# Performance work log

Measured on AMD Instinct MI355X. Metric: run time of the kernel, lower is better.

## Reference

```python
import jax, jax.numpy as jnp
import numpy as np

N_NODES = 50000

# DGL ChebConv with k=2 and the standard lambda_max=2 approximation:
#   L_hat = L - I = -D^{-1/2} A D^{-1/2}
#   X0 = X ; X1 = L_hat @ X ; out = concat([X0, X1], -1) @ W + b
# Norm uses in-degrees (DGL behavior).

def setup_inputs() -> dict:
    key = jax.random.key(0)
    ks = jax.random.split(key, 8)
    E = 800000
    src = jax.random.randint(ks[0], (E,), 0, N_NODES, dtype=jnp.int32)
    dst = jax.random.randint(ks[1], (E,), 0, N_NODES, dtype=jnp.int32)
    def w(k, shape):
        fan_in = shape[0]
        return jax.random.normal(k, shape, jnp.float32) * (1.0 / np.sqrt(fan_in))
    return {
        "x": jax.random.normal(ks[2], (N_NODES, 128), jnp.float32),
        "src": src, "dst": dst,
        "W1": w(ks[3], (256, 256)), "b1": jnp.zeros((256,), jnp.float32),
        "W2": w(ks[4], (512, 256)), "b2": jnp.zeros((256,), jnp.float32),
        "W3": w(ks[5], (512, 128)), "b3": jnp.zeros((128,), jnp.float32),
    }

def _cheb_layer(h, src, dst, dinv, W, b):
    # X1 = -D^{-1/2} A D^{-1/2} h  (lambda_max = 2)
    hn = h * dinv[:, None]
    agg = jax.ops.segment_sum(hn[src], dst, num_segments=N_NODES)
    x1 = -(agg * dinv[:, None])
    return jnp.concatenate([h, x1], axis=-1) @ W + b

def reference(x, src, dst, W1, b1, W2, b2, W3, b3):
    deg = jax.ops.segment_sum(jnp.ones_like(dst, dtype=x.dtype), dst,
                              num_segments=N_NODES)
    dinv = jnp.where(deg > 0, jax.lax.rsqrt(jnp.maximum(deg, 1.0)), 0.0)
    h = jnp.tanh(_cheb_layer(x, src, dst, dinv, W1, b1))
    for _ in range(3):  # hid_layer = 3
        h = jnp.tanh(_cheb_layer(h, src, dst, dinv, W2, b2))
    return _cheb_layer(h, src, dst, dinv, W3, b3)
```

## Files before the change

kernel.cpp:

```cpp
#include <hip/hip_runtime.h>
#include <cmath>

#define NN 50000
#define CAP 64

typedef short v8s __attribute__((ext_vector_type(8)));
typedef float v4f __attribute__((ext_vector_type(4)));

__device__ __forceinline__ float b2f(unsigned short u) {
    return __uint_as_float(((unsigned int)u) << 16);
}
__device__ __forceinline__ unsigned short f2b(float f) {
    unsigned int x = __float_as_uint(f);
    x += 0x7fffu + ((x >> 16) & 1u);
    return (unsigned short)(x >> 16);
}

__device__ __forceinline__ void gld16(const void* g, void* l) {
    __builtin_amdgcn_global_load_lds(
        (const __attribute__((address_space(1))) unsigned int*)g,
        (__attribute__((address_space(3))) unsigned int*)l, 16, 0, 0);
}

__global__ void sniff_kernel(const unsigned short* __restrict__ x, int* __restrict__ mode) {
    if (threadIdx.x == 0 && blockIdx.x == 0) {
        int c = 0;
        for (int i = 0; i < 128; ++i) {
            unsigned int e = (x[i] >> 7) & 0xFFu;
            if (e >= 100u && e <= 140u) ++c;
        }
        *mode = (c >= 112) ? 0 : 1;
    }
}

__global__ void fill_kernel(const int* __restrict__ src, const int* __restrict__ dst,
                            int* __restrict__ cnt, unsigned short* __restrict__ ell, int E) {
    int e = blockIdx.x * blockDim.x + threadIdx.x;
    if (e < E) {
        int d = dst[e];
        int pos = atomicAdd(&cnt[d], 1);
        if (pos < CAP) ell[d * CAP + pos] = (unsigned short)src[e];
    }
}

__global__ void dinv_kernel(const int* __restrict__ cnt, float* __restrict__ dinv, int n) {
    int i = blockIdx.x * blockDim.x + threadIdx.x;
    if (i < n) {
        int d = cnt[i];
        dinv[i] = (d > 0) ? rsqrtf((float)d) : 0.0f;
    }
}

__global__ void prep_kernel(const void* __restrict__ x,
                            const void* __restrict__ W1, const void* __restrict__ W2,
                            const void* __restrict__ W3, const void* __restrict__ b1,
                            const void* __restrict__ b2, const void* __restrict__ b3,
                            unsigned short* __restrict__ buf,
                            unsigned short* __restrict__ WT1, unsigned short* __restrict__ WT2,
                            unsigned short* __restrict__ WT3, unsigned short* __restrict__ bb1,
                            unsigned short* __restrict__ bb2, unsigned short* __restrict__ bb3,
                            const int* __restrict__ modep) {
    int mode = *modep;
    int b = blockIdx.x, t = threadIdx.x;
    if (b < 3125) {
        int idx = b * 256 + t;
        int n = idx >> 4, c = idx & 15;
        if (mode == 0) {
            ((uint4*)buf)[n * 64 + c] = ((const uint4*)x)[idx];
        } else {
            const float* xf = (const float*)x + (size_t)idx * 8;
            unsigned short o[8];
#pragma unroll
            for (int i = 0; i < 8; ++i) o[i] = f2b(xf[i]);
            ((uint4*)buf)[n * 64 + c] = *(const uint4*)o;
        }
    } else if (b < 3381) {
        int idx = (b - 3125) * 256 + t;
        int n = idx >> 8, k = idx & 255;
        WT1[idx] = mode ? f2b(((const float*)W1)[k * 256 + n])
                        : ((const unsigned short*)W1)[k * 256 + n];
    } else if (b < 3893) {
        int idx = (b - 3381) * 256 + t;
        int n = idx >> 9, k = idx & 511;
        WT2[idx] = mode ? f2b(((const float*)W2)[k * 256 + n])
                        : ((const unsigned short*)W2)[k * 256 + n];
    } else if (b < 4149) {
        int idx = (b - 3893) * 256 + t;
        int n = idx >> 9, k = idx & 511;
        WT3[idx] = mode ? f2b(((const float*)W3)[k * 128 + n])
                        : ((const unsigned short*)W3)[k * 128 + n];
    } else {
        if (t < 256) {
            bb1[t] = mode ? f2b(((const float*)b1)[t]) : ((const unsigned short*)b1)[t];
            bb2[t] = mode ? f2b(((const float*)b2)[t]) : ((const unsigned short*)b2)[t];
        }
        if (t < 128)
            bb3[t] = mode ? f2b(((const float*)b3)[t]) : ((const unsigned short*)b3)[t];
    }
}

template <int FPL>
__global__ void spmm_kernel(const unsigned short* __restrict__ h, int ldh,
                            const int* __restrict__ cnt, const unsigned short* __restrict__ ell,
                            const float* __restrict__ dinv,
                            unsigned short* __restrict__ out, int ldo) {
    int node = blockIdx.x * 4 + (threadIdx.x >> 6);
    int lane = threadIdx.x & 63;
    int c = cnt[node]; c = (c < CAP) ? c : CAP;
    int sl = (int)ell[node * CAP + lane];
    float dl = dinv[sl];
    float acc[FPL];
#pragma unroll
    for (int i = 0; i < FPL; ++i) acc[i] = 0.f;
    const int col = lane * FPL;

    int g = 0;
    for (; g + 8 <= c; g += 8) {
        int s[8]; float d[8];
#pragma unroll
        for (int i = 0; i < 8; ++i) { s[i] = __shfl(sl, g + i); d[i] = __shfl(dl, g + i); }
        if (FPL == 4) {
            ushort4 v[8];
#pragma unroll
            for (int i = 0; i < 8; ++i)
                v[i] = *(const ushort4*)(h + (size_t)s[i] * ldh + col);
#pragma unroll
            for (int i = 0; i < 8; ++i) {
                acc[0] += d[i] * b2f(v[i].x); acc[1] += d[i] * b2f(v[i].y);
                acc[2] += d[i] * b2f(v[i].z); acc[3] += d[i] * b2f(v[i].w);
            }
        } else {
            ushort2 v[8];
#pragma unroll
            for (int i = 0; i < 8; ++i)
                v[i] = *(const ushort2*)(h + (size_t)s[i] * ldh + col);
#pragma unroll
            for (int i = 0; i < 8; ++i) {
                acc[0] += d[i] * b2f(v[i].x); acc[1] += d[i] * b2f(v[i].y);
            }
        }
    }
    for (; g < c; ++g) {
        int sg = __shfl(sl, g);
        float dg = __shfl(dl, g);
        const unsigned short* hp = h + (size_t)sg * ldh + col;
        if (FPL == 4) {
            ushort4 v = *(const ushort4*)hp;
            acc[0] += dg * b2f(v.x); acc[1] += dg * b2f(v.y);
            acc[2] += dg * b2f(v.z); acc[3] += dg * b2f(v.w);
        } else {
            ushort2 v = *(const ushort2*)hp;
            acc[0] += dg * b2f(v.x); acc[1] += dg * b2f(v.y);
        }
    }

    float dn = -dinv[node];
    unsigned short* op = out + (size_t)node * ldo + col;
    if (FPL == 4) {
        ushort4 o;
        o.x = f2b(acc[0] * dn); o.y = f2b(acc[1] * dn);
        o.z = f2b(acc[2] * dn); o.w = f2b(acc[3] * dn);
        *(ushort4*)op = o;
    } else {
        ushort2 o;
        o.x = f2b(acc[0] * dn); o.y = f2b(acc[1] * dn);
        *(ushort2*)op = o;
    }
}

template <int K32, int NQ>
__global__ void gemm_lds_kernel(const unsigned short* __restrict__ A, int lda,
                                const unsigned short* __restrict__ WT,
                                const unsigned short* __restrict__ bias,
                                void* __restrict__ out, int ldo,
                                int M, int dotanh, int is_final, const int* __restrict__ modep) {
    constexpr int K    = K32 * 32;
    constexpr int NB   = NQ * 64;
    constexpr int NTHR = 2 * NQ * 64;
    constexpr int ACH  = 128 * 4;
    constexpr int BCH  = NB * 4;
    constexpr int ROUNDS = (ACH + BCH) / NTHR;
    __shared__ unsigned short lds[(128 + NB) * 32];

    const int tid = threadIdx.x;
    const int wave = tid >> 6, lane = tid & 63, quad = lane >> 4, l16 = lane & 15;
    const int mh = wave / NQ, nq = wave % NQ;
    const int m0 = blockIdx.x * 128;

    v4f acc[4][4];
#pragma unroll
    for (int mi = 0; mi < 4; ++mi)
#pragma unroll
        for (int ni = 0; ni < 4; ++ni) acc[mi][ni] = (v4f){0.f, 0.f, 0.f, 0.f};

    const unsigned short* gp[ROUNDS];
#pragma unroll
    for (int r = 0; r < ROUNDS; ++r) {
        int c = tid + r * NTHR;
        if (c < ACH) {
            int row = m0 + (c >> 2);
            if (row >= M) row = M - 1;
            gp[r] = A + (size_t)row * lda + (c & 3) * 8;
        } else {
            int cb = c - ACH;
            gp[r] = WT + (size_t)(cb >> 2) * K + (cb & 3) * 8;
        }
    }

    const unsigned short* aT = lds;
    const unsigned short* bT = lds + 128 * 32;

    for (int k0 = 0; k0 < K; k0 += 32) {
#pragma unroll
        for (int r = 0; r < ROUNDS; ++r) {
            int c = tid + r * NTHR;
            gld16(gp[r] + k0, (void*)&lds[c * 8]);
        }
        __syncthreads();

        v8s a_frag[4], b_frag[4];
#pragma unroll
        for (int mi = 0; mi < 4; ++mi)
            a_frag[mi] = *(const v8s*)&aT[(mh * 64 + mi * 16 + l16) * 32 + quad * 8];
#pragma unroll
        for (int ni = 0; ni < 4; ++ni)
            b_frag[ni] = *(const v8s*)&bT[(nq * 64 + ni * 16 + l16) * 32 + quad * 8];
#pragma unroll
        for (int mi = 0; mi < 4; ++mi)
#pragma unroll
            for (int ni = 0; ni < 4; ++ni)
                acc[mi][ni] = __builtin_amdgcn_mfma_f32_16x16x32_bf16(a_frag[mi], b_frag[ni],
                                                                      acc[mi][ni], 0, 0, 0);
        __syncthreads();
    }

    int fin = is_final ? *modep : 0;
#pragma unroll
    for (int ni = 0; ni < 4; ++ni) {
        int colc = nq * 64 + ni * 16 + l16;
        float bv = b2f(bias[colc]);
#pragma unroll
        for (int mi = 0; mi < 4; ++mi) {
#pragma unroll
            for (int r = 0; r < 4; ++r) {
                int row = m0 + mh * 64 + mi * 16 + quad * 4 + r;
                if (row < M) {
                    float v = acc[mi][ni][r] + bv;
                    if (dotanh) v = tanhf(v);
                    if (fin) ((float*)out)[(size_t)row * ldo + colc] = v;
                    else     ((unsigned short*)out)[(size_t)row * ldo + colc] = f2b(v);
                }
            }
        }
    }
}

static inline size_t al256(size_t x) { return (x + 255) & ~(size_t)255; }

extern "C" void kernel_launch(void* const* d_in, const int* in_sizes, int n_in,
                              void* d_out, int out_size, void* d_ws, size_t ws_size,
                              hipStream_t stream) {
    const void* x  = d_in[0];
    const int* src = (const int*)d_in[1];
    const int* dst = (const int*)d_in[2];
    const void* W1 = d_in[3]; const void* b1 = d_in[4];
    const void* W2 = d_in[5]; const void* b2 = d_in[6];
    const void* W3 = d_in[7]; const void* b3 = d_in[8];
    const int E = in_sizes[1];

    char* p = (char*)d_ws;
    int* mode     = (int*)p;            p += 256;
    int* cnt      = (int*)p;            p += al256((size_t)NN * 4);
    float* dinv   = (float*)p;          p += al256((size_t)NN * 4);
    unsigned short* ell = (unsigned short*)p; p += al256((size_t)NN * CAP * 2);
    unsigned short* WT1 = (unsigned short*)p; p += al256((size_t)256 * 256 * 2);
    unsigned short* WT2 = (unsigned short*)p; p += al256((size_t)256 * 512 * 2);
    unsigned short* WT3 = (unsigned short*)p; p += al256((size_t)128 * 512 * 2);
    unsigned short* bb1 = (unsigned short*)p; p += al256((size_t)256 * 2);
    unsigned short* bb2 = (unsigned short*)p; p += al256((size_t)256 * 2);
    unsigned short* bb3 = (unsigned short*)p; p += al256((size_t)128 * 2);
    unsigned short* buf = (unsigned short*)p; p += al256((size_t)NN * 512 * 2);

    hipMemsetAsync(cnt, 0, (size_t)NN * 4, stream);
    sniff_kernel<<<1, 64, 0, stream>>>((const unsigned short*)x, mode);
    prep_kernel<<<4150, 256, 0, stream>>>(x, W1, W2, W3, b1, b2, b3,
                                          buf, WT1, WT2, WT3, bb1, bb2, bb3, mode);
    int eb = (E + 255) / 256;
    fill_kernel<<<eb, 256, 0, stream>>>(src, dst, cnt, ell, E);
    dinv_kernel<<<(NN + 255) / 256, 256, 0, stream>>>(cnt, dinv, NN);

    const int SPMM_GRID = NN / 4;
    const int GB = (NN + 127) / 128;

    spmm_kernel<2><<<SPMM_GRID, 256, 0, stream>>>(buf, 512, cnt, ell, dinv, buf + 128, 512);
    gemm_lds_kernel<8, 4><<<GB, 512, 0, stream>>>(buf, 512, WT1, bb1, buf, 512, NN, 1, 0, mode);
    spmm_kernel<4><<<SPMM_GRID, 256, 0, stream>>>(buf, 512, cnt, ell, dinv, buf + 256, 512);
    gemm_lds_kernel<16, 4><<<GB, 512, 0, stream>>>(buf, 512, WT2, bb2, buf, 512, NN, 1, 0, mode);
    spmm_kernel<4><<<SPMM_GRID, 256, 0, stream>>>(buf, 512, cnt, ell, dinv, buf + 256, 512);
    gemm_lds_kernel<16, 4><<<GB, 512, 0, stream>>>(buf, 512, WT2, bb2, buf, 512, NN, 1, 0, mode);
    spmm_kernel<4><<<SPMM_GRID, 256, 0, stream>>>(buf, 512, cnt, ell, dinv, buf + 256, 512);
    gemm_lds_kernel<16, 4><<<GB, 512, 0, stream>>>(buf, 512, WT2, bb2, buf, 512, NN, 1, 0, mode);
    spmm_kernel<4><<<SPMM_GRID, 256, 0, stream>>>(buf, 512, cnt, ell, dinv, buf + 256, 512);
    gemm_lds_kernel<16, 2><<<GB, 256, 0, stream>>>(buf, 512, WT3, bb3, d_out, 128, NN, 0, 1, mode);
}
```

Before: 555.6 us.

## Split SpMM across column slices and drop LDS staging in GEMM

The SpMM now launches several blocks per node group, each handling a 32-column slice. Lanes are split into four edge groups with a shuffle reduction at the end, which gives more parallelism and narrower gathers per block. The GEMM drops LDS staging via global_load_lds and the per-k-step barriers. Each wave now loads its MFMA fragments straight from global memory into registers, with smaller 256-thread blocks and a 64-row tile for the hidden layers. This trades LDS reuse across waves for fewer syncs, and it risks redundant global and L2 traffic since each wave reloads B and A fragments.

```diff
diff --git a/kernel.cpp b/kernel.cpp
--- a/kernel.cpp
+++ b/kernel.cpp
@@ -14,12 +14,6 @@
     unsigned int x = __float_as_uint(f);
     x += 0x7fffu + ((x >> 16) & 1u);
     return (unsigned short)(x >> 16);
-}
-
-__device__ __forceinline__ void gld16(const void* g, void* l) {
-    __builtin_amdgcn_global_load_lds(
-        (const __attribute__((address_space(1))) unsigned int*)g,
-        (__attribute__((address_space(3))) unsigned int*)l, 16, 0, 0);
 }
 
 __global__ void sniff_kernel(const unsigned short* __restrict__ x, int* __restrict__ mode) {
@@ -99,93 +93,66 @@
     }
 }
 
-template <int FPL>
-__global__ void spmm_kernel(const unsigned short* __restrict__ h, int ldh,
-                            const int* __restrict__ cnt, const unsigned short* __restrict__ ell,
+template <int NS, int OBASE>
+__global__ void spmm_kernel(const unsigned short* __restrict__ h,
+                            const int* __restrict__ cnt,
+                            const unsigned short* __restrict__ ell,
                             const float* __restrict__ dinv,
-                            unsigned short* __restrict__ out, int ldo) {
-    int node = blockIdx.x * 4 + (threadIdx.x >> 6);
-    int lane = threadIdx.x & 63;
+                            unsigned short* __restrict__ out) {
+    const int s = blockIdx.x % NS;
+    const int node = (blockIdx.x / NS) * 4 + (threadIdx.x >> 6);
+    const int lane = threadIdx.x & 63;
+    const int e = lane >> 4, cp = lane & 15;
     int c = cnt[node]; c = (c < CAP) ? c : CAP;
-    int sl = (int)ell[node * CAP + lane];
-    float dl = dinv[sl];
-    float acc[FPL];
-#pragma unroll
-    for (int i = 0; i < FPL; ++i) acc[i] = 0.f;
-    const int col = lane * FPL;
-
-    int g = 0;
-    for (; g + 8 <= c; g += 8) {
-        int s[8]; float d[8];
-#pragma unroll
-        for (int i = 0; i < 8; ++i) { s[i] = __shfl(sl, g + i); d[i] = __shfl(dl, g + i); }
-        if (FPL == 4) {
-            ushort4 v[8];
-#pragma unroll
-            for (int i = 0; i < 8; ++i)
-                v[i] = *(const ushort4*)(h + (size_t)s[i] * ldh + col);
-#pragma unroll
-            for (int i = 0; i < 8; ++i) {
-                acc[0] += d[i] * b2f(v[i].x); acc[1] += d[i] * b2f(v[i].y);
-                acc[2] += d[i] * b2f(v[i].z); acc[3] += d[i] * b2f(v[i].w);
-            }
-        } else {
-            ushort2 v[8];
-#pragma unroll
-            for (int i = 0; i < 8; ++i)
-                v[i] = *(const ushort2*)(h + (size_t)s[i] * ldh + col);
-#pragma unroll
-            for (int i = 0; i < 8; ++i) {
-                acc[0] += d[i] * b2f(v[i].x); acc[1] += d[i] * b2f(v[i].y);
-            }
-        }
-    }
-    for (; g < c; ++g) {
-        int sg = __shfl(sl, g);
-        float dg = __shfl(dl, g);
-        const unsigned short* hp = h + (size_t)sg * ldh + col;
-        if (FPL == 4) {
-            ushort4 v = *(const ushort4*)hp;
-            acc[0] += dg * b2f(v.x); acc[1] += dg * b2f(v.y);
-            acc[2] += dg * b2f(v.z); acc[3] += dg * b2f(v.w);
-        } else {
-            ushort2 v = *(const ushort2*)hp;
-            acc[0] += dg * b2f(v.x); acc[1] += dg * b2f(v.y);
-        }
-    }
-
-    float dn = -dinv[node];
-    unsigned short* op = out + (size_t)node * ldo + col;
-    if (FPL == 4) {
-        ushort4 o;
-        o.x = f2b(acc[0] * dn); o.y = f2b(acc[1] * dn);
-        o.z = f2b(acc[2] * dn); o.w = f2b(acc[3] * dn);
-        *(ushort4*)op = o;
-    } else {
-        ushort2 o;
-        o.x = f2b(acc[0] * dn); o.y = f2b(acc[1] * dn);
-        *(ushort2*)op = o;
-    }
-}
-
-template <int K32, int NQ>
-__global__ void gemm_lds_kernel(const unsigned short* __restrict__ A, int lda,
-                                const unsigned short* __restrict__ WT,
-                                const unsigned short* __restrict__ bias,
-                                void* __restrict__ out, int ldo,
-                                int M, int dotanh, int is_final, const int* __restrict__ modep) {
-    constexpr int K    = K32 * 32;
-    constexpr int NB   = NQ * 64;
-    constexpr int NTHR = 2 * NQ * 64;
-    constexpr int ACH  = 128 * 4;
-    constexpr int BCH  = NB * 4;
-    constexpr int ROUNDS = (ACH + BCH) / NTHR;
-    __shared__ unsigned short lds[(128 + NB) * 32];
-
+    int sl = 0; float dl = 0.f;
+    if (lane < c) { sl = (int)ell[node * CAP + lane]; dl = dinv[sl]; }
+    const int colb = s * 32 + cp * 2;
+    float a0 = 0.f, a1 = 0.f;
+    const int cpad = (c + 7) & ~7;
+    for (int g = 0; g < cpad; g += 8) {
+        int i0 = g + e, i1 = g + 4 + e;
+        int s0 = __shfl(sl, i0), s1 = __shfl(sl, i1);
+        float d0 = __shfl(dl, i0), d1 = __shfl(dl, i1);
+        ushort2 v0 = *(const ushort2*)(h + (size_t)s0 * 512 + colb);
+        ushort2 v1 = *(const ushort2*)(h + (size_t)s1 * 512 + colb);
+        a0 += d0 * b2f(v0.x) + d1 * b2f(v1.x);
+        a1 += d0 * b2f(v0.y) + d1 * b2f(v1.y);
+    }
+    a0 += __shfl_xor(a0, 16); a0 += __shfl_xor(a0, 32);
+    a1 += __shfl_xor(a1, 16); a1 += __shfl_xor(a1, 32);
+    if (lane < 16) {
+        float dn = -dinv[node];
+        ushort2 o; o.x = f2b(a0 * dn); o.y = f2b(a1 * dn);
+        *(ushort2*)(out + (size_t)node * 512 + OBASE + colb) = o;
+    }
+}
+
+template <int K32, int NT>
+__global__ __launch_bounds__(256) void gemm_kernel(
+        const unsigned short* __restrict__ A, int lda,
+        const unsigned short* __restrict__ WT,
+        const unsigned short* __restrict__ bias,
+        void* __restrict__ out, int ldo,
+        int M, int dotanh, int is_final, const int* __restrict__ modep) {
+    constexpr int K = K32 * 32;
+    constexpr int RPB = (4 / NT) * 64;
     const int tid = threadIdx.x;
     const int wave = tid >> 6, lane = tid & 63, quad = lane >> 4, l16 = lane & 15;
-    const int mh = wave / NQ, nq = wave % NQ;
-    const int m0 = blockIdx.x * 128;
+    const int mrow = wave / NT, nq = wave % NT;
+    const int m0 = blockIdx.x * RPB + mrow * 64;
+    const int n0 = nq * 64;
+
+    const unsigned short* Ap[4];
+#pragma unroll
+    for (int mi = 0; mi < 4; ++mi) {
+        int r = m0 + mi * 16 + l16;
+        if (r >= M) r = M - 1;
+        Ap[mi] = A + (size_t)r * lda + quad * 8;
+    }
+    const unsigned short* Bp[4];
+#pragma unroll
+    for (int ni = 0; ni < 4; ++ni)
+        Bp[ni] = WT + (size_t)(n0 + ni * 16 + l16) * K + quad * 8;
 
     v4f acc[4][4];
 #pragma unroll
@@ -193,57 +160,33 @@
 #pragma unroll
         for (int ni = 0; ni < 4; ++ni) acc[mi][ni] = (v4f){0.f, 0.f, 0.f, 0.f};
 
-    const unsigned short* gp[ROUNDS];
-#pragma unroll
-    for (int r = 0; r < ROUNDS; ++r) {
-        int c = tid + r * NTHR;
-        if (c < ACH) {
-            int row = m0 + (c >> 2);
-            if (row >= M) row = M - 1;
-            gp[r] = A + (size_t)row * lda + (c & 3) * 8;
-        } else {
-            int cb = c - ACH;
-            gp[r] = WT + (size_t)(cb >> 2) * K + (cb & 3) * 8;
-        }
-    }
-
-    const unsigned short* aT = lds;
-    const unsigned short* bT = lds + 128 * 32;
-
-    for (int k0 = 0; k0 < K; k0 += 32) {
-#pragma unroll
-        for (int r = 0; r < ROUNDS; ++r) {
-            int c = tid + r * NTHR;
-            gld16(gp[r] + k0, (void*)&lds[c * 8]);
-        }
-        __syncthreads();
-
-        v8s a_frag[4], b_frag[4];
+#pragma unroll 2
+    for (int j = 0; j < K32; ++j) {
+        v8s a[4], b[4];
+#pragma unroll
+        for (int mi = 0; mi < 4; ++mi) a[mi] = *(const v8s*)(Ap[mi] + j * 32);
+#pragma unroll
+        for (int ni = 0; ni < 4; ++ni) b[ni] = *(const v8s*)(Bp[ni] + j * 32);
 #pragma unroll
         for (int mi = 0; mi < 4; ++mi)
-            a_frag[mi] = *(const v8s*)&aT[(mh * 64 + mi * 16 + l16) * 32 + quad * 8];
-#pragma unroll
-        for (int ni = 0; ni < 4; ++ni)
-            b_frag[ni] = *(const v8s*)&bT[(nq * 64 + ni * 16 + l16) * 32 + quad * 8];
-#pragma unroll
-        for (int mi = 0; mi < 4; ++mi)
 #pragma unroll
             for (int ni = 0; ni < 4; ++ni)
-                acc[mi][ni] = __builtin_amdgcn_mfma_f32_16x16x32_bf16(a_frag[mi], b_frag[ni],
+                acc[mi][ni] = __builtin_amdgcn_mfma_f32_16x16x32_bf16(a[mi], b[ni],
                                                                       acc[mi][ni], 0, 0, 0);
-        __syncthreads();
-    }
+    }
+
+    __syncthreads();
 
     int fin = is_final ? *modep : 0;
 #pragma unroll
     for (int ni = 0; ni < 4; ++ni) {
-        int colc = nq * 64 + ni * 16 + l16;
+        int colc = n0 + ni * 16 + l16;
         float bv = b2f(bias[colc]);
 #pragma unroll
         for (int mi = 0; mi < 4; ++mi) {
 #pragma unroll
             for (int r = 0; r < 4; ++r) {
-                int row = m0 + mh * 64 + mi * 16 + quad * 4 + r;
+                int row = m0 + mi * 16 + quad * 4 + r;
                 if (row < M) {
                     float v = acc[mi][ni][r] + bv;
                     if (dotanh) v = tanhf(v);
@@ -289,17 +232,19 @@
     fill_kernel<<<eb, 256, 0, stream>>>(src, dst, cnt, ell, E);
     dinv_kernel<<<(NN + 255) / 256, 256, 0, stream>>>(cnt, dinv, NN);
 
-    const int SPMM_GRID = NN / 4;
-    const int GB = (NN + 127) / 128;
-
-    spmm_kernel<2><<<SPMM_GRID, 256, 0, stream>>>(buf, 512, cnt, ell, dinv, buf + 128, 512);
-    gemm_lds_kernel<8, 4><<<GB, 512, 0, stream>>>(buf, 512, WT1, bb1, buf, 512, NN, 1, 0, mode);
-    spmm_kernel<4><<<SPMM_GRID, 256, 0, stream>>>(buf, 512, cnt, ell, dinv, buf + 256, 512);
-    gemm_lds_kernel<16, 4><<<GB, 512, 0, stream>>>(buf, 512, WT2, bb2, buf, 512, NN, 1, 0, mode);
-    spmm_kernel<4><<<SPMM_GRID, 256, 0, stream>>>(buf, 512, cnt, ell, dinv, buf + 256, 512);
-    gemm_lds_kernel<16, 4><<<GB, 512, 0, stream>>>(buf, 512, WT2, bb2, buf, 512, NN, 1, 0, mode);
-    spmm_kernel<4><<<SPMM_GRID, 256, 0, stream>>>(buf, 512, cnt, ell, dinv, buf + 256, 512);
-    gemm_lds_kernel<16, 4><<<GB, 512, 0, stream>>>(buf, 512, WT2, bb2, buf, 512, NN, 1, 0, mode);
-    spmm_kernel<4><<<SPMM_GRID, 256, 0, stream>>>(buf, 512, cnt, ell, dinv, buf + 256, 512);
-    gemm_lds_kernel<16, 2><<<GB, 256, 0, stream>>>(buf, 512, WT3, bb3, d_out, 128, NN, 0, 1, mode);
-}
+    const int SG1 = 4 * (NN / 4);
+    const int SG  = 8 * (NN / 4);
+    const int GB4 = (NN + 63) / 64;
+    const int GB2 = (NN + 127) / 128;
+
+    spmm_kernel<4, 128><<<SG1, 256, 0, stream>>>(buf, cnt, ell, dinv, buf);
+    gemm_kernel<8, 4><<<GB4, 256, 0, stream>>>(buf, 512, WT1, bb1, buf, 512, NN, 1, 0, mode);
+    spmm_kernel<8, 256><<<SG, 256, 0, stream>>>(buf, cnt, ell, dinv, buf);
+    gemm_kernel<16, 4><<<GB4, 256, 0, stream>>>(buf, 512, WT2, bb2, buf, 512, NN, 1, 0, mode);
+    spmm_kernel<8, 256><<<SG, 256, 0, stream>>>(buf, cnt, ell, dinv, buf);
+    gemm_kernel<16, 4><<<GB4, 256, 0, stream>>>(buf, 512, WT2, bb2, buf, 512, NN, 1, 0, mode);
+    spmm_kernel<8, 256><<<SG, 256, 0, stream>>>(buf, cnt, ell, dinv, buf);
+    gemm_kernel<16, 4><<<GB4, 256, 0, stream>>>(buf, 512, WT2, bb2, buf, 512, NN, 1, 0, mode);
+    spmm_kernel<8, 256><<<SG, 256, 0, stream>>>(buf, cnt, ell, dinv, buf);
+    gemm_kernel<16, 2><<<GB2, 256, 0, stream>>>(buf, 512, WT3, bb3, d_out, 128, NN, 0, 1, mode);
+}
```

Result: slower. 1.073 ms (+93.1%).

## Stage full-K A rows in padded LDS and stream weights directly from global

Applied to the files above, without the earlier changes.

Replaces the k-stepped LDS GEMM with one that loads a 64-row block of A across the whole K dimension into padded LDS once, with a single barrier. Each wave then reads its B fragments straight from global memory (L2/L1-cached weights) instead of staging them in LDS. The M tile drops from 128 to 64 rows and each wave owns a 64-column slice. This removes the per-k-step barriers and the async global-to-LDS copies. In exchange the grid doubles, each weight fragment is re-read from cache by more blocks, and the LDS footprint grows for K=512, which may limit occupancy.

```diff
diff --git a/kernel.cpp b/kernel.cpp
--- a/kernel.cpp
+++ b/kernel.cpp
@@ -14,12 +14,6 @@
     unsigned int x = __float_as_uint(f);
     x += 0x7fffu + ((x >> 16) & 1u);
     return (unsigned short)(x >> 16);
-}
-
-__device__ __forceinline__ void gld16(const void* g, void* l) {
-    __builtin_amdgcn_global_load_lds(
-        (const __attribute__((address_space(1))) unsigned int*)g,
-        (__attribute__((address_space(3))) unsigned int*)l, 16, 0, 0);
 }
 
 __global__ void sniff_kernel(const unsigned short* __restrict__ x, int* __restrict__ mode) {
@@ -168,82 +162,73 @@
     }
 }
 
-template <int K32, int NQ>
-__global__ void gemm_lds_kernel(const unsigned short* __restrict__ A, int lda,
-                                const unsigned short* __restrict__ WT,
-                                const unsigned short* __restrict__ bias,
-                                void* __restrict__ out, int ldo,
-                                int M, int dotanh, int is_final, const int* __restrict__ modep) {
+template <int K32, int NT>
+__global__ void gemm_kernel(
+        const unsigned short* __restrict__ A, int lda,
+        const unsigned short* __restrict__ WT,
+        const unsigned short* __restrict__ bias,
+        void* __restrict__ out, int ldo,
+        int M, int dotanh, int is_final, const int* __restrict__ modep) {
     constexpr int K    = K32 * 32;
-    constexpr int NB   = NQ * 64;
-    constexpr int NTHR = 2 * NQ * 64;
-    constexpr int ACH  = 128 * 4;
-    constexpr int BCH  = NB * 4;
-    constexpr int ROUNDS = (ACH + BCH) / NTHR;
-    __shared__ unsigned short lds[(128 + NB) * 32];
+    constexpr int LDK  = K + 8;
+    constexpr int NTHR = NT * 64;
+    constexpr int CPR  = K / 8;
+    constexpr int ROUNDS = 64 * CPR / NTHR;
+    __shared__ unsigned short aT[64 * LDK];
 
     const int tid = threadIdx.x;
     const int wave = tid >> 6, lane = tid & 63, quad = lane >> 4, l16 = lane & 15;
-    const int mh = wave / NQ, nq = wave % NQ;
-    const int m0 = blockIdx.x * 128;
-
-    v4f acc[4][4];
-#pragma unroll
-    for (int mi = 0; mi < 4; ++mi)
-#pragma unroll
-        for (int ni = 0; ni < 4; ++ni) acc[mi][ni] = (v4f){0.f, 0.f, 0.f, 0.f};
-
-    const unsigned short* gp[ROUNDS];
+    const int m0 = blockIdx.x * 64;
+    const int n0 = wave * 64;
+
 #pragma unroll
     for (int r = 0; r < ROUNDS; ++r) {
         int c = tid + r * NTHR;
-        if (c < ACH) {
-            int row = m0 + (c >> 2);
-            if (row >= M) row = M - 1;
-            gp[r] = A + (size_t)row * lda + (c & 3) * 8;
-        } else {
-            int cb = c - ACH;
-            gp[r] = WT + (size_t)(cb >> 2) * K + (cb & 3) * 8;
-        }
-    }
-
-    const unsigned short* aT = lds;
-    const unsigned short* bT = lds + 128 * 32;
-
-    for (int k0 = 0; k0 < K; k0 += 32) {
-#pragma unroll
-        for (int r = 0; r < ROUNDS; ++r) {
-            int c = tid + r * NTHR;
-            gld16(gp[r] + k0, (void*)&lds[c * 8]);
-        }
-        __syncthreads();
-
-        v8s a_frag[4], b_frag[4];
+        int row = c / CPR, ko = (c % CPR) * 8;
+        int grow = m0 + row;
+        if (grow >= M) grow = M - 1;
+        v8s v = *(const v8s*)(A + (size_t)grow * lda + ko);
+        *(v8s*)&aT[row * LDK + ko] = v;
+    }
+    __syncthreads();
+
+    const unsigned short* Bp[4];
+#pragma unroll
+    for (int ni = 0; ni < 4; ++ni)
+        Bp[ni] = WT + (size_t)(n0 + ni * 16 + l16) * K + quad * 8;
+
+    v4f acc[4][4];
+#pragma unroll
+    for (int mi = 0; mi < 4; ++mi)
+#pragma unroll
+        for (int ni = 0; ni < 4; ++ni) acc[mi][ni] = (v4f){0.f, 0.f, 0.f, 0.f};
+
+#pragma unroll 4
+    for (int j = 0; j < K32; ++j) {
+        v8s a[4], b[4];
+#pragma unroll
+        for (int ni = 0; ni < 4; ++ni) b[ni] = *(const v8s*)(Bp[ni] + j * 32);
 #pragma unroll
         for (int mi = 0; mi < 4; ++mi)
-            a_frag[mi] = *(const v8s*)&aT[(mh * 64 + mi * 16 + l16) * 32 + quad * 8];
-#pragma unroll
-        for (int ni = 0; ni < 4; ++ni)
-            b_frag[ni] = *(const v8s*)&bT[(nq * 64 + ni * 16 + l16) * 32 + quad * 8];
+            a[mi] = *(const v8s*)&aT[(mi * 16 + l16) * LDK + j * 32 + quad * 8];
 #pragma unroll
         for (int mi = 0; mi < 4; ++mi)
 #pragma unroll
             for (int ni = 0; ni < 4; ++ni)
-                acc[mi][ni] = __builtin_amdgcn_mfma_f32_16x16x32_bf16(a_frag[mi], b_frag[ni],
+                acc[mi][ni] = __builtin_amdgcn_mfma_f32_16x16x32_bf16(a[mi], b[ni],
                                                                       acc[mi][ni], 0, 0, 0);
-        __syncthreads();
     }
 
     int fin = is_final ? *modep : 0;
 #pragma unroll
     for (int ni = 0; ni < 4; ++ni) {
-        int colc = nq * 64 + ni * 16 + l16;
+        int colc = n0 + ni * 16 + l16;
         float bv = b2f(bias[colc]);
 #pragma unroll
         for (int mi = 0; mi < 4; ++mi) {
 #pragma unroll
             for (int r = 0; r < 4; ++r) {
-                int row = m0 + mh * 64 + mi * 16 + quad * 4 + r;
+                int row = m0 + mi * 16 + quad * 4 + r;
                 if (row < M) {
                     float v = acc[mi][ni][r] + bv;
                     if (dotanh) v = tanhf(v);
@@ -290,16 +275,16 @@
     dinv_kernel<<<(NN + 255) / 256, 256, 0, stream>>>(cnt, dinv, NN);
 
     const int SPMM_GRID = NN / 4;
-    const int GB = (NN + 127) / 128;
+    const int GB = (NN + 63) / 64;
 
     spmm_kernel<2><<<SPMM_GRID, 256, 0, stream>>>(buf, 512, cnt, ell, dinv, buf + 128, 512);
-    gemm_lds_kernel<8, 4><<<GB, 512, 0, stream>>>(buf, 512, WT1, bb1, buf, 512, NN, 1, 0, mode);
-    spmm_kernel<4><<<SPMM_GRID, 256, 0, stream>>>(buf, 512, cnt, ell, dinv, buf + 256, 512);
-    gemm_lds_kernel<16, 4><<<GB, 512, 0, stream>>>(buf, 512, WT2, bb2, buf, 512, NN, 1, 0, mode);
-    spmm_kernel<4><<<SPMM_GRID, 256, 0, stream>>>(buf, 512, cnt, ell, dinv, buf + 256, 512);
-    gemm_lds_kernel<16, 4><<<GB, 512, 0, stream>>>(buf, 512, WT2, bb2, buf, 512, NN, 1, 0, mode);
-    spmm_kernel<4><<<SPMM_GRID, 256, 0, stream>>>(buf, 512, cnt, ell, dinv, buf + 256, 512);
-    gemm_lds_kernel<16, 4><<<GB, 512, 0, stream>>>(buf, 512, WT2, bb2, buf, 512, NN, 1, 0, mode);
-    spmm_kernel<4><<<SPMM_GRID, 256, 0, stream>>>(buf, 512, cnt, ell, dinv, buf + 256, 512);
-    gemm_lds_kernel<16, 2><<<GB, 256, 0, stream>>>(buf, 512, WT3, bb3, d_out, 128, NN, 0, 1, mode);
-}
+    gemm_kernel<8, 4><<<GB, 256, 0, stream>>>(buf, 512, WT1, bb1, buf, 512, NN, 1, 0, mode);
+    spmm_kernel<4><<<SPMM_GRID, 256, 0, stream>>>(buf, 512, cnt, ell, dinv, buf + 256, 512);
+    gemm_kernel<16, 4><<<GB, 256, 0, stream>>>(buf, 512, WT2, bb2, buf, 512, NN, 1, 0, mode);
+    spmm_kernel<4><<<SPMM_GRID, 256, 0, stream>>>(buf, 512, cnt, ell, dinv, buf + 256, 512);
+    gemm_kernel<16, 4><<<GB, 256, 0, stream>>>(buf, 512, WT2, bb2, buf, 512, NN, 1, 0, mode);
+    spmm_kernel<4><<<SPMM_GRID, 256, 0, stream>>>(buf, 512, cnt, ell, dinv, buf + 256, 512);
+    gemm_kernel<16, 4><<<GB, 256, 0, stream>>>(buf, 512, WT2, bb2, buf, 512, NN, 1, 0, mode);
+    spmm_kernel<4><<<SPMM_GRID, 256, 0, stream>>>(buf, 512, cnt, ell, dinv, buf + 256, 512);
+    gemm_kernel<16, 2><<<GB, 128, 0, stream>>>(buf, 512, WT3, bb3, d_out, 128, NN, 0, 1, mode);
+}
```

Measured after the change: 744.4 us. 34.0% more time.
